# Performance work log

Measured on AMD Instinct MI355X. Metric: run time of the kernel, lower is better.

The kernel has to match this reference:

```python
import jax, jax.numpy as jnp
import numpy as np

T, B = 128, 512
IN = 512          # input_size = prod(observation_shape)
H = 1024          # hidden size
NA = 256          # n_actions
IDX0 = jnp.arange(0, 128)    # sub_indices[0]
IDX1 = jnp.arange(128, 256)  # sub_indices[1]


def _mlp(x, w1, b1, w2, b2, w3, b3):
    h = jnp.tanh(x @ w1.T + b1)
    h = jnp.tanh(h @ w2.T + b2)
    return h @ w3.T + b3


def _linear_init(key, out_dim, in_dim):
    kw, kb = jax.random.split(key)
    s = 1.0 / np.sqrt(in_dim)
    w = jax.random.uniform(kw, (out_dim, in_dim), jnp.float32, -s, s)
    b = jax.random.uniform(kb, (out_dim,), jnp.float32, -s, s)
    return w, b


def setup_inputs() -> dict:
    key = jax.random.key(0)
    ks = jax.random.split(key, 12)
    # observation: [T,B,IN+3]; last 3 dims are the routing gate features
    core = jax.random.normal(ks[0], (T, B, IN), jnp.float32)
    gate = jax.random.uniform(ks[1], (T, B, 3), jnp.float32, -0.2, 0.2)
    obs = jnp.concatenate([core, gate], axis=-1)
    pf_w1, pf_b1 = _linear_init(ks[2], H, IN)
    pf_w2, pf_b2 = _linear_init(ks[3], H, H)
    pf_w3, pf_b3 = _linear_init(ks[4], 128, H)
    pc_w1, pc_b1 = _linear_init(ks[5], H, IN)
    pc_w2, pc_b2 = _linear_init(ks[6], H, H)
    pc_w3, pc_b3 = _linear_init(ks[7], 128, H)
    v_w1, v_b1 = _linear_init(ks[8], H, IN)
    v_w2, v_b2 = _linear_init(ks[9], H, H)
    v_w3, v_b3 = _linear_init(ks[10], 1, H)
    return dict(
        observation=obs,
        prev_action=jnp.zeros((T, B), jnp.int32),
        prev_reward=jnp.zeros((T, B), jnp.float32),
        pf_w1=pf_w1, pf_b1=pf_b1, pf_w2=pf_w2, pf_b2=pf_b2, pf_w3=pf_w3, pf_b3=pf_b3,
        pc_w1=pc_w1, pc_b1=pc_b1, pc_w2=pc_w2, pc_b2=pc_b2, pc_w3=pc_w3, pc_b3=pc_b3,
        v_w1=v_w1, v_b1=v_b1, v_w2=v_w2, v_b2=v_b2, v_w3=v_w3, v_b3=v_b3,
    )


def reference(observation, prev_action, prev_reward,
              pf_w1, pf_b1, pf_w2, pf_b2, pf_w3, pf_b3,
              pc_w1, pc_b1, pc_w2, pc_b2, pc_w3, pc_b3,
              v_w1, v_b1, v_w2, v_b2, v_w3, v_b3):
    obs_flat = observation.reshape(T * B, -1)      # [TB, IN+3]
    x = obs_flat[:, :IN]                            # [TB, IN]
    # routing: free expert iff all 3 gate features have |.| <= 0.1
    mask = jnp.all(jnp.abs(obs_flat[:, IN:IN + 3]) <= 0.1, axis=-1)  # [TB]
    p_free = jax.nn.softmax(_mlp(x, pf_w1, pf_b1, pf_w2, pf_b2, pf_w3, pf_b3), axis=-1)
    p_con = jax.nn.softmax(_mlp(x, pc_w1, pc_b1, pc_w2, pc_b2, pc_w3, pc_b3), axis=-1)
    zeros = jnp.zeros((T * B, NA), x.dtype)
    pi_free = zeros.at[:, IDX0].set(p_free)
    pi_con = zeros.at[:, IDX1].set(p_con)
    pi = jnp.where(mask[:, None], pi_free, pi_con)  # [TB, NA]
    v = _mlp(x, v_w1, v_b1, v_w2, v_b2, v_w3, v_b3).squeeze(-1)  # [TB]
    return pi.reshape(T, B, NA), v.reshape(T, B)
```

## Files before the change

### kernel.cpp

```cpp
#include <hip/hip_runtime.h>
#include <stdint.h>

#define M_TOTAL 65536
#define IN_DIM 512
#define OBS_DIM 515

typedef __bf16 bf16x8 __attribute__((ext_vector_type(8)));
typedef float f32x4 __attribute__((ext_vector_type(4)));
typedef unsigned short u16x8 __attribute__((ext_vector_type(8)));

__device__ __forceinline__ unsigned short f2bf(float f) {
  unsigned u = __float_as_uint(f);
  u = (u + 0x7FFFu + ((u >> 16) & 1u)) >> 16;
  return (unsigned short)u;
}
__device__ __forceinline__ float bf2f(unsigned short h) {
  return __uint_as_float(((unsigned)h) << 16);
}
__device__ __forceinline__ float fast_tanh(float z) {
  float e = __expf(2.0f * z);
  return 1.0f - 2.0f / (e + 1.0f);
}
__device__ __forceinline__ void gl16(const void* g, void* l) {
  __builtin_amdgcn_global_load_lds(
      (__attribute__((address_space(1))) void*)g,
      (__attribute__((address_space(3))) void*)l, 16, 0, 0);
}

struct P8 { const float* p[8]; };

__global__ __launch_bounds__(256) void fused_cast(
    P8 srcs, unsigned short* __restrict__ dst, int* __restrict__ cnt) {
  if (blockIdx.x == 0 && threadIdx.x < 128) cnt[threadIdx.x] = 0;
  const int b0 = 524288, b1 = 1048576, b2 = 1572864, b3 = 2621440,
            b4 = 3670016, b5 = 4718592, b6 = 4849664, b7 = 4980736;
  int stride = gridDim.x * 256;
  for (int i = blockIdx.x * 256 + threadIdx.x; i < b7; i += stride) {
    const float* s; int off;
    if (i < b2)      { if (i < b0) { s = srcs.p[0]; off = i; }
                       else if (i < b1) { s = srcs.p[1]; off = i - b0; }
                       else { s = srcs.p[2]; off = i - b1; } }
    else if (i < b5) { if (i < b3) { s = srcs.p[3]; off = i - b2; }
                       else if (i < b4) { s = srcs.p[4]; off = i - b3; }
                       else { s = srcs.p[5]; off = i - b4; } }
    else             { if (i < b6) { s = srcs.p[6]; off = i - b5; }
                       else { s = srcs.p[7]; off = i - b6; } }
    dst[i] = f2bf(s[off]);
  }
}

__global__ __launch_bounds__(256) void compact_kernel(
    const float* __restrict__ obs,
    int* __restrict__ cntF, int* __restrict__ cntC,
    int* __restrict__ idxF, int* __restrict__ idxC, int C) {
  __shared__ int lcF, lcC, baseF, baseC;
  const int tid = threadIdx.x;
  const int r = blockIdx.x * 256 + tid;
  const float* g = obs + (size_t)r * OBS_DIM + IN_DIM;
  bool m = (fabsf(g[0]) <= 0.1f) && (fabsf(g[1]) <= 0.1f) && (fabsf(g[2]) <= 0.1f);
  if (tid == 0) { lcF = 0; lcC = 0; }
  __syncthreads();
  int slot = m ? atomicAdd(&lcF, 1) : atomicAdd(&lcC, 1);
  __syncthreads();
  const int c = r / C;
  if (tid == 0) {
    baseF = atomicAdd(&cntF[c], lcF);
    baseC = atomicAdd(&cntC[c], lcC);
  }
  __syncthreads();
  const int local = r - c * C;
  if (m) idxF[(size_t)c * C + baseF + slot] = local;
  else   idxC[(size_t)c * C + baseC + slot] = local;
}

__global__ __launch_bounds__(256) void build_idxP(
    const int* __restrict__ cntF, const int* __restrict__ cntC,
    const int* __restrict__ idxF, const int* __restrict__ idxC,
    int* __restrict__ idxP, int* __restrict__ meta, int C, int Cp) {
  const int bpc = Cp >> 8;
  const int c = blockIdx.x / bpc;
  const int i = (blockIdx.x % bpc) * 256 + threadIdx.x;
  const int cf = cntF[c], cc = cntC[c];
  const int padF = (cf + 127) & ~127;
  const int total = padF + ((cc + 127) & ~127);
  if ((blockIdx.x % bpc) == 0 && threadIdx.x == 0) {
    meta[2 * c] = padF; meta[2 * c + 1] = total;
  }
  if (i >= total) return;
  int v;
  if (i < padF) v = idxF[(size_t)c * C + (i < cf ? i : 0)];
  else { int j = i - padF; v = idxC[(size_t)c * C + (j < cc ? j : 0)]; }
  idxP[(size_t)c * Cp + i] = v;
}

__global__ __launch_bounds__(256) void prep_x(
    const float* __restrict__ obs, unsigned short* __restrict__ x, int row0) {
  int g = blockIdx.x * 256 + threadIdx.x;
  int row = g >> 9, col = g & 511;
  x[g] = f2bf(obs[(size_t)(row0 + row) * OBS_DIM + col]);
}

__global__ __launch_bounds__(256) void gemm_bt_tanh(
    const unsigned short* __restrict__ A, int lda,
    const unsigned short* __restrict__ B,
    const float* __restrict__ bias,
    unsigned short* __restrict__ Cmat, int ldc, int K)
{
  __shared__ alignas(16) unsigned short sA[128 * 32];
  __shared__ alignas(16) unsigned short sB[128 * 32];
  const int tid = threadIdx.x;
  const int nx = gridDim.x;
  const int nwg = nx * gridDim.y;
  const int orig = blockIdx.y * nx + blockIdx.x;
  const int wg = (orig & 7) * (nwg >> 3) + (orig >> 3);
  const int n0 = (wg % nx) << 7;
  const int m0 = (wg / nx) << 7;

  const int lane = tid & 63;
  const int wv = tid >> 6;
  const int wm = wv >> 1, wn = wv & 1;
  const int lr = lane & 15;
  const int lk = lane >> 4;

  const int ar0 = tid >> 2, ar1 = (256 + tid) >> 2;
  const int acol = (tid & 3) << 3;
  const unsigned short* Ap0 = A + (size_t)(m0 + ar0) * lda + acol;
  const unsigned short* Ap1 = A + (size_t)(m0 + ar1) * lda + acol;
  const unsigned short* Bp0 = B + (size_t)(n0 + ar0) * K + acol;
  const unsigned short* Bp1 = B + (size_t)(n0 + ar1) * K + acol;
  const int du = (tid & ~63) << 3;

  const f32x4 zero = {0.f, 0.f, 0.f, 0.f};
  f32x4 acc[4][4];
#pragma unroll
  for (int i = 0; i < 4; ++i)
#pragma unroll
    for (int j = 0; j < 4; ++j) acc[i][j] = zero;

  for (int kt = 0; kt < K; kt += 32) {
    __syncthreads();
    gl16(Ap0 + kt, &sA[du]);
    gl16(Bp0 + kt, &sB[du]);
    gl16(Ap1 + kt, &sA[du + 2048]);
    gl16(Bp1 + kt, &sB[du + 2048]);
    __syncthreads();
    bf16x8 af[4], bfr[4];
#pragma unroll
    for (int i = 0; i < 4; ++i)
      af[i] = *(const bf16x8*)&sA[((wm << 6) + (i << 4) + lr) * 32 + (lk << 3)];
#pragma unroll
    for (int j = 0; j < 4; ++j)
      bfr[j] = *(const bf16x8*)&sB[((wn << 6) + (j << 4) + lr) * 32 + (lk << 3)];
#pragma unroll
    for (int i = 0; i < 4; ++i)
#pragma unroll
      for (int j = 0; j < 4; ++j)
        acc[i][j] = __builtin_amdgcn_mfma_f32_16x16x32_bf16(af[i], bfr[j], acc[i][j], 0, 0, 0);
  }

  const int crow = m0 + (wm << 6);
  const int ccol = n0 + (wn << 6);
#pragma unroll
  for (int j = 0; j < 4; ++j) {
    int col = ccol + (j << 4) + lr;
    float bv = bias[col];
#pragma unroll
    for (int i = 0; i < 4; ++i) {
#pragma unroll
      for (int r = 0; r < 4; ++r) {
        int row = crow + (i << 4) + (lk << 2) + r;
        Cmat[(size_t)row * ldc + col] = f2bf(fast_tanh(acc[i][j][r] + bv));
      }
    }
  }
}

__global__ __launch_bounds__(256) void gemm_bt_tanh_p(
    const unsigned short* __restrict__ A, int lda,
    const unsigned short* __restrict__ BF, const unsigned short* __restrict__ BC,
    const float* __restrict__ biasF, const float* __restrict__ biasC,
    unsigned short* __restrict__ Cmat, int ldc, int K,
    const int* __restrict__ idxP, const int* __restrict__ meta)
{
  __shared__ alignas(16) unsigned short sA[128 * 32];
  __shared__ alignas(16) unsigned short sB[128 * 32];
  __shared__ int s_idx[128];
  const int tid = threadIdx.x;
  const int nx = gridDim.x;
  const int nwg = nx * gridDim.y;
  const int orig = blockIdx.y * nx + blockIdx.x;
  const int wg = (orig & 7) * (nwg >> 3) + (orig >> 3);
  const int n0 = (wg % nx) << 7;
  const int m0 = (wg / nx) << 7;

  const int padF = meta[0], total = meta[1];
  if (m0 >= total) return;
  const unsigned short* B = (m0 < padF) ? BF : BC;
  const float* bias = (m0 < padF) ? biasF : biasC;
  if (idxP && tid < 128) s_idx[tid] = idxP[m0 + tid];
  __syncthreads();

  const int lane = tid & 63;
  const int wv = tid >> 6;
  const int wm = wv >> 1, wn = wv & 1;
  const int lr = lane & 15;
  const int lk = lane >> 4;

  const int ar0 = tid >> 2, ar1 = (256 + tid) >> 2;
  const int acol = (tid & 3) << 3;
  const int ga0 = idxP ? s_idx[ar0] : (m0 + ar0);
  const int ga1 = idxP ? s_idx[ar1] : (m0 + ar1);
  const unsigned short* Ap0 = A + (size_t)ga0 * lda + acol;
  const unsigned short* Ap1 = A + (size_t)ga1 * lda + acol;
  const unsigned short* Bp0 = B + (size_t)(n0 + ar0) * K + acol;
  const unsigned short* Bp1 = B + (size_t)(n0 + ar1) * K + acol;
  const int du = (tid & ~63) << 3;

  const f32x4 zero = {0.f, 0.f, 0.f, 0.f};
  f32x4 acc[4][4];
#pragma unroll
  for (int i = 0; i < 4; ++i)
#pragma unroll
    for (int j = 0; j < 4; ++j) acc[i][j] = zero;

  for (int kt = 0; kt < K; kt += 32) {
    __syncthreads();
    gl16(Ap0 + kt, &sA[du]);
    gl16(Bp0 + kt, &sB[du]);
    gl16(Ap1 + kt, &sA[du + 2048]);
    gl16(Bp1 + kt, &sB[du + 2048]);
    __syncthreads();
    bf16x8 af[4], bfr[4];
#pragma unroll
    for (int i = 0; i < 4; ++i)
      af[i] = *(const bf16x8*)&sA[((wm << 6) + (i << 4) + lr) * 32 + (lk << 3)];
#pragma unroll
    for (int j = 0; j < 4; ++j)
      bfr[j] = *(const bf16x8*)&sB[((wn << 6) + (j << 4) + lr) * 32 + (lk << 3)];
#pragma unroll
    for (int i = 0; i < 4; ++i)
#pragma unroll
      for (int j = 0; j < 4; ++j)
        acc[i][j] = __builtin_amdgcn_mfma_f32_16x16x32_bf16(af[i], bfr[j], acc[i][j], 0, 0, 0);
  }

  const int crow = m0 + (wm << 6);
  const int ccol = n0 + (wn << 6);
#pragma unroll
  for (int j = 0; j < 4; ++j) {
    int col = ccol + (j << 4) + lr;
    float bv = bias[col];
#pragma unroll
    for (int i = 0; i < 4; ++i) {
#pragma unroll
      for (int r = 0; r < 4; ++r) {
        int row = crow + (i << 4) + (lk << 2) + r;
        Cmat[(size_t)row * ldc + col] = f2bf(fast_tanh(acc[i][j][r] + bv));
      }
    }
  }
}

__global__ __launch_bounds__(256) void l3_policy_p(
    const unsigned short* __restrict__ H2,
    const unsigned short* __restrict__ W3F, const unsigned short* __restrict__ W3C,
    const float* __restrict__ b3F, const float* __restrict__ b3C,
    const int* __restrict__ idxP, const int* __restrict__ meta,
    float* __restrict__ out_pi, int row0)
{
  __shared__ alignas(16) unsigned short sA[128 * 32];
  __shared__ alignas(16) unsigned short sB[128 * 32];
  __shared__ int s_idx[128];
  const int tid = threadIdx.x;
  const int m0 = blockIdx.x << 7;
  const int padF = meta[0], total = meta[1];
  if (m0 >= total) return;
  const bool freeg = (m0 < padF);
  const unsigned short* W3 = freeg ? W3F : W3C;
  const float* b3 = freeg ? b3F : b3C;
  const int half = freeg ? 0 : 128;
  if (tid < 128) s_idx[tid] = idxP[m0 + tid];
  __syncthreads();

  const int lane = tid & 63;
  const int wv = tid >> 6;
  const int lr = lane & 15;
  const int lk = lane >> 4;

  const int ar0 = tid >> 2, ar1 = (256 + tid) >> 2;
  const int acol = (tid & 3) << 3;
  const unsigned short* Ap0 = H2 + (size_t)(m0 + ar0) * 1024 + acol;
  const unsigned short* Ap1 = H2 + (size_t)(m0 + ar1) * 1024 + acol;
  const unsigned short* Bp0 = W3 + (size_t)ar0 * 1024 + acol;
  const unsigned short* Bp1 = W3 + (size_t)ar1 * 1024 + acol;
  const int du = (tid & ~63) << 3;

  const f32x4 zero = {0.f, 0.f, 0.f, 0.f};
  f32x4 acc[2][8];
#pragma unroll
  for (int i = 0; i < 2; ++i)
#pragma unroll
    for (int j = 0; j < 8; ++j) acc[i][j] = zero;

  for (int kt = 0; kt < 1024; kt += 32) {
    __syncthreads();
    gl16(Ap0 + kt, &sA[du]);
    gl16(Bp0 + kt, &sB[du]);
    gl16(Ap1 + kt, &sA[du + 2048]);
    gl16(Bp1 + kt, &sB[du + 2048]);
    __syncthreads();
    bf16x8 af[2], bfr[8];
#pragma unroll
    for (int i = 0; i < 2; ++i)
      af[i] = *(const bf16x8*)&sA[((wv << 5) + (i << 4) + lr) * 32 + (lk << 3)];
#pragma unroll
    for (int j = 0; j < 8; ++j)
      bfr[j] = *(const bf16x8*)&sB[((j << 4) + lr) * 32 + (lk << 3)];
#pragma unroll
    for (int i = 0; i < 2; ++i)
#pragma unroll
      for (int j = 0; j < 8; ++j)
        acc[i][j] = __builtin_amdgcn_mfma_f32_16x16x32_bf16(af[i], bfr[j], acc[i][j], 0, 0, 0);
  }

  float bv[8];
#pragma unroll
  for (int j = 0; j < 8; ++j) bv[j] = b3[(j << 4) + lr];

#pragma unroll
  for (int i = 0; i < 2; ++i) {
#pragma unroll
    for (int r = 0; r < 4; ++r) {
      float lg[8];
      float mx = -3.4e38f;
#pragma unroll
      for (int j = 0; j < 8; ++j) { lg[j] = acc[i][j][r] + bv[j]; mx = fmaxf(mx, lg[j]); }
#pragma unroll
      for (int d = 1; d < 16; d <<= 1) mx = fmaxf(mx, __shfl_xor(mx, d));
      float s = 0.f;
#pragma unroll
      for (int j = 0; j < 8; ++j) { lg[j] = __expf(lg[j] - mx); s += lg[j]; }
#pragma unroll
      for (int d = 1; d < 16; d <<= 1) s += __shfl_xor(s, d);
      float inv = 1.f / s;
      int compact = m0 + (wv << 5) + (i << 4) + (lk << 2) + r;
      int grow = row0 + s_idx[compact - m0];
      size_t base = (size_t)grow * 256;
#pragma unroll
      for (int j = 0; j < 8; ++j)
        out_pi[base + half + (j << 4) + lr] = lg[j] * inv;
#pragma unroll
      for (int j = 0; j < 8; ++j)
        out_pi[base + (half ^ 128) + (j << 4) + lr] = 0.0f;
    }
  }
}

__global__ __launch_bounds__(256) void l3_value(
    const unsigned short* __restrict__ H2,
    const float* __restrict__ w3,
    const float* __restrict__ b3,
    float* __restrict__ out_v, int row0, int C)
{
  const int lane = threadIdx.x & 63;
  const int row = (blockIdx.x << 2) + (threadIdx.x >> 6);
  if (row >= C) return;
  float s = 0.f;
#pragma unroll
  for (int it = 0; it < 2; ++it) {
    int k = (it << 9) + (lane << 3);
    u16x8 h = *(const u16x8*)(H2 + (size_t)row * 1024 + k);
    const float4* wp = (const float4*)(w3 + k);
    float4 w0 = wp[0], w1 = wp[1];
    s += bf2f(h[0]) * w0.x + bf2f(h[1]) * w0.y + bf2f(h[2]) * w0.z + bf2f(h[3]) * w0.w;
    s += bf2f(h[4]) * w1.x + bf2f(h[5]) * w1.y + bf2f(h[6]) * w1.z + bf2f(h[7]) * w1.w;
  }
#pragma unroll
  for (int d = 1; d < 64; d <<= 1) s += __shfl_xor(s, d);
  if (lane == 0) out_v[row0 + row] = s + b3[0];
}

extern "C" void kernel_launch(void* const* d_in, const int* in_sizes, int n_in,
                              void* d_out, int out_size, void* d_ws, size_t ws_size,
                              hipStream_t stream)
{
  (void)in_sizes; (void)n_in; (void)out_size;
  const float* obs   = (const float*)d_in[0];
  const float* pf_w1 = (const float*)d_in[3];
  const float* pf_b1 = (const float*)d_in[4];
  const float* pf_w2 = (const float*)d_in[5];
  const float* pf_b2 = (const float*)d_in[6];
  const float* pf_w3 = (const float*)d_in[7];
  const float* pf_b3 = (const float*)d_in[8];
  const float* pc_w1 = (const float*)d_in[9];
  const float* pc_b1 = (const float*)d_in[10];
  const float* pc_w2 = (const float*)d_in[11];
  const float* pc_b2 = (const float*)d_in[12];
  const float* pc_w3 = (const float*)d_in[13];
  const float* pc_b3 = (const float*)d_in[14];
  const float* v_w1  = (const float*)d_in[15];
  const float* v_b1  = (const float*)d_in[16];
  const float* v_w2  = (const float*)d_in[17];
  const float* v_b2  = (const float*)d_in[18];
  const float* v_w3  = (const float*)d_in[19];
  const float* v_b3  = (const float*)d_in[20];

  float* out_pi = (float*)d_out;
  float* out_v  = out_pi + (size_t)M_TOTAL * 256;

  char* ws = (char*)d_ws;
  unsigned short* wPF1 = (unsigned short*)ws;
  unsigned short* wPC1 = wPF1 + 524288;
  unsigned short* wV1  = wPC1 + 524288;
  unsigned short* wPF2 = wV1  + 524288;
  unsigned short* wPC2 = wPF2 + 1048576;
  unsigned short* wV2  = wPC2 + 1048576;
  unsigned short* wPF3 = wV2  + 1048576;
  unsigned short* wPC3 = wPF3 + 131072;
  int* cntF = (int*)(wPC3 + 131072);
  int* cntC = cntF + 64;
  int* idxF = cntC + 64;
  int* idxC = idxF + 65536;
  int* meta = idxC + 65536;
  int* idxP = meta + 128;
  unsigned short* xb = (unsigned short*)(idxP + 81920);

  const size_t fixed = (size_t)9961472 + 4 * (64 + 64 + 65536 + 65536 + 128 + 81920);
  int C = 1024;
  if      (ws_size >= fixed + 5120ull * 65536 + 1048576) C = 65536;
  else if (ws_size >= fixed + 5120ull * 32768 + 1048576) C = 32768;
  else if (ws_size >= fixed + 5120ull * 16384 + 1048576) C = 16384;
  else if (ws_size >= fixed + 5120ull *  8192 + 1048576) C = 8192;
  else if (ws_size >= fixed + 5120ull *  4096 + 1048576) C = 4096;
  else if (ws_size >= fixed + 5120ull *  2048 + 1048576) C = 2048;
  const int nchunk = M_TOTAL / C;
  const int Cp = C + 256;

  unsigned short* h1p = xb + (size_t)C * 512;
  unsigned short* h2p = h1p + (size_t)Cp * 1024;

  P8 srcs;
  srcs.p[0] = pf_w1; srcs.p[1] = pc_w1; srcs.p[2] = v_w1;
  srcs.p[3] = pf_w2; srcs.p[4] = pc_w2; srcs.p[5] = v_w2;
  srcs.p[6] = pf_w3; srcs.p[7] = pc_w3;
  fused_cast<<<2048, 256, 0, stream>>>(srcs, wPF1, cntF);
  compact_kernel<<<M_TOTAL / 256, 256, 0, stream>>>(obs, cntF, cntC, idxF, idxC, C);
  build_idxP<<<nchunk * (Cp / 256), 256, 0, stream>>>(cntF, cntC, idxF, idxC, idxP, meta, C, Cp);

  const dim3 gv(8, C / 128);
  const dim3 gp(8, Cp / 128);
  for (int c = 0; c < nchunk; ++c) {
    int row0 = c * C;
    prep_x<<<C * 512 / 256, 256, 0, stream>>>(obs, xb, row0);
    gemm_bt_tanh<<<gv, 256, 0, stream>>>(xb, 512, wV1, v_b1, h1p, 1024, 512);
    gemm_bt_tanh<<<gv, 256, 0, stream>>>(h1p, 1024, wV2, v_b2, h2p, 1024, 1024);
    l3_value<<<C / 4, 256, 0, stream>>>(h2p, v_w3, v_b3, out_v, row0, C);
    gemm_bt_tanh_p<<<gp, 256, 0, stream>>>(xb, 512, wPF1, wPC1, pf_b1, pc_b1,
                                           h1p, 1024, 512, idxP + (size_t)c * Cp, meta + 2 * c);
    gemm_bt_tanh_p<<<gp, 256, 0, stream>>>(h1p, 1024, wPF2, wPC2, pf_b2, pc_b2,
                                           h2p, 1024, 1024, nullptr, meta + 2 * c);
    l3_policy_p<<<Cp / 128, 256, 0, stream>>>(h2p, wPF3, wPC3, pf_b3, pc_b3,
                                              idxP + (size_t)c * Cp, meta + 2 * c, out_pi, row0);
  }
}
```

Baseline: 834.1 us.

## Replace 128x128 GEMMs with double-buffered 256x256 tile kernel using swizzled LDS

Both GEMM kernels are replaced by a single 512-thread kernel that computes 256x256 output tiles with a 64-wide K step. It double-buffers global-to-LDS loads across quarter-iterations, uses an XOR-swizzled LDS layout, and raises MFMA priority. Expert padding moves from 128 to 256 rows to match the larger tile. The aim is more data reuse per load and overlap of memory traffic with MFMA work. The cost is 128KB of LDS per block, which lowers occupancy, plus extra padded rows of wasted work.

```diff
diff --git a/kernel.cpp b/kernel.cpp
--- a/kernel.cpp
+++ b/kernel.cpp
@@ -81,8 +81,8 @@
   const int c = blockIdx.x / bpc;
   const int i = (blockIdx.x % bpc) * 256 + threadIdx.x;
   const int cf = cntF[c], cc = cntC[c];
-  const int padF = (cf + 127) & ~127;
-  const int total = padF + ((cc + 127) & ~127);
+  const int padF = (cf + 255) & ~255;
+  const int total = padF + ((cc + 255) & ~255);
   if ((blockIdx.x % bpc) == 0 && threadIdx.x == 0) {
     meta[2 * c] = padF; meta[2 * c + 1] = total;
   }
@@ -100,163 +100,157 @@
   x[g] = f2bf(obs[(size_t)(row0 + row) * OBS_DIM + col]);
 }
 
-__global__ __launch_bounds__(256) void gemm_bt_tanh(
-    const unsigned short* __restrict__ A, int lda,
-    const unsigned short* __restrict__ B,
-    const float* __restrict__ bias,
-    unsigned short* __restrict__ Cmat, int ldc, int K)
-{
-  __shared__ alignas(16) unsigned short sA[128 * 32];
-  __shared__ alignas(16) unsigned short sB[128 * 32];
-  const int tid = threadIdx.x;
-  const int nx = gridDim.x;
-  const int nwg = nx * gridDim.y;
-  const int orig = blockIdx.y * nx + blockIdx.x;
-  const int wg = (orig & 7) * (nwg >> 3) + (orig >> 3);
-  const int n0 = (wg % nx) << 7;
-  const int m0 = (wg / nx) << 7;
-
-  const int lane = tid & 63;
-  const int wv = tid >> 6;
-  const int wm = wv >> 1, wn = wv & 1;
-  const int lr = lane & 15;
-  const int lk = lane >> 4;
-
-  const int ar0 = tid >> 2, ar1 = (256 + tid) >> 2;
-  const int acol = (tid & 3) << 3;
-  const unsigned short* Ap0 = A + (size_t)(m0 + ar0) * lda + acol;
-  const unsigned short* Ap1 = A + (size_t)(m0 + ar1) * lda + acol;
-  const unsigned short* Bp0 = B + (size_t)(n0 + ar0) * K + acol;
-  const unsigned short* Bp1 = B + (size_t)(n0 + ar1) * K + acol;
-  const int du = (tid & ~63) << 3;
-
-  const f32x4 zero = {0.f, 0.f, 0.f, 0.f};
-  f32x4 acc[4][4];
-#pragma unroll
-  for (int i = 0; i < 4; ++i)
-#pragma unroll
-    for (int j = 0; j < 4; ++j) acc[i][j] = zero;
-
-  for (int kt = 0; kt < K; kt += 32) {
-    __syncthreads();
-    gl16(Ap0 + kt, &sA[du]);
-    gl16(Bp0 + kt, &sB[du]);
-    gl16(Ap1 + kt, &sA[du + 2048]);
-    gl16(Bp1 + kt, &sB[du + 2048]);
-    __syncthreads();
-    bf16x8 af[4], bfr[4];
-#pragma unroll
-    for (int i = 0; i < 4; ++i)
-      af[i] = *(const bf16x8*)&sA[((wm << 6) + (i << 4) + lr) * 32 + (lk << 3)];
-#pragma unroll
-    for (int j = 0; j < 4; ++j)
-      bfr[j] = *(const bf16x8*)&sB[((wn << 6) + (j << 4) + lr) * 32 + (lk << 3)];
-#pragma unroll
-    for (int i = 0; i < 4; ++i)
-#pragma unroll
-      for (int j = 0; j < 4; ++j)
-        acc[i][j] = __builtin_amdgcn_mfma_f32_16x16x32_bf16(af[i], bfr[j], acc[i][j], 0, 0, 0);
-  }
-
-  const int crow = m0 + (wm << 6);
-  const int ccol = n0 + (wn << 6);
-#pragma unroll
-  for (int j = 0; j < 4; ++j) {
-    int col = ccol + (j << 4) + lr;
-    float bv = bias[col];
-#pragma unroll
-    for (int i = 0; i < 4; ++i) {
-#pragma unroll
-      for (int r = 0; r < 4; ++r) {
-        int row = crow + (i << 4) + (lk << 2) + r;
-        Cmat[(size_t)row * ldc + col] = f2bf(fast_tanh(acc[i][j][r] + bv));
-      }
-    }
-  }
-}
-
-__global__ __launch_bounds__(256) void gemm_bt_tanh_p(
+#define STAGE_A(h, tt, db) { \
+    const unsigned short* _s = pA[h] + (size_t)(tt) * 64 + grp8; \
+    char* _d = smem + (db) * 65536 + (h) * 16384 + wbase; \
+    gl16(_s, _d); gl16(_s + 32, _d + 8192); }
+#define STAGE_B(h, tt, db) { \
+    const unsigned short* _s = pB[h] + (size_t)(tt) * 64 + grp8; \
+    char* _d = smem + (db) * 65536 + 32768 + (h) * 16384 + wbase; \
+    gl16(_s, _d); gl16(_s + 32, _d + 8192); }
+
+__global__ __launch_bounds__(512) void gemm256(
     const unsigned short* __restrict__ A, int lda,
     const unsigned short* __restrict__ BF, const unsigned short* __restrict__ BC,
     const float* __restrict__ biasF, const float* __restrict__ biasC,
     unsigned short* __restrict__ Cmat, int ldc, int K,
-    const int* __restrict__ idxP, const int* __restrict__ meta)
+    const int* __restrict__ idxP, const int* __restrict__ meta, int Mrows)
 {
-  __shared__ alignas(16) unsigned short sA[128 * 32];
-  __shared__ alignas(16) unsigned short sB[128 * 32];
-  __shared__ int s_idx[128];
+  extern __shared__ char smem[];
   const int tid = threadIdx.x;
-  const int nx = gridDim.x;
-  const int nwg = nx * gridDim.y;
-  const int orig = blockIdx.y * nx + blockIdx.x;
-  const int wg = (orig & 7) * (nwg >> 3) + (orig >> 3);
-  const int n0 = (wg % nx) << 7;
-  const int m0 = (wg / nx) << 7;
-
-  const int padF = meta[0], total = meta[1];
+
+  const int nwg = gridDim.x * gridDim.y;
+  const int orig = blockIdx.y * gridDim.x + blockIdx.x;
+  const int qq = nwg >> 3, rr = nwg & 7, xc = orig & 7, oo = orig >> 3;
+  const int wg = (xc < rr ? xc * (qq + 1) : rr * (qq + 1) + (xc - rr) * qq) + oo;
+  const int n0 = (wg % gridDim.x) << 8;
+  const int m0 = (wg / gridDim.x) << 8;
+
+  const int padF  = meta ? meta[0] : (1 << 30);
+  const int total = meta ? meta[1] : Mrows;
   if (m0 >= total) return;
   const unsigned short* B = (m0 < padF) ? BF : BC;
   const float* bias = (m0 < padF) ? biasF : biasC;
-  if (idxP && tid < 128) s_idx[tid] = idxP[m0 + tid];
-  __syncthreads();
 
   const int lane = tid & 63;
   const int wv = tid >> 6;
-  const int wm = wv >> 1, wn = wv & 1;
+  const int wm = wv >> 2, wn = wv & 3;
   const int lr = lane & 15;
   const int lk = lane >> 4;
 
-  const int ar0 = tid >> 2, ar1 = (256 + tid) >> 2;
-  const int acol = (tid & 3) << 3;
-  const int ga0 = idxP ? s_idx[ar0] : (m0 + ar0);
-  const int ga1 = idxP ? s_idx[ar1] : (m0 + ar1);
-  const unsigned short* Ap0 = A + (size_t)ga0 * lda + acol;
-  const unsigned short* Ap1 = A + (size_t)ga1 * lda + acol;
-  const unsigned short* Bp0 = B + (size_t)(n0 + ar0) * K + acol;
-  const unsigned short* Bp1 = B + (size_t)(n0 + ar1) * K + acol;
-  const int du = (tid & ~63) << 3;
+  const int srow = tid >> 2;
+  const int grp8 = (((tid & 3) ^ ((srow >> 1) & 3)) << 3);
+  const int wbase = (tid & ~63) << 4;
+  const unsigned short* pA[2];
+  const unsigned short* pB[2];
+#pragma unroll
+  for (int h = 0; h < 2; ++h) {
+    int gr = m0 + h * 128 + srow;
+    int ga = idxP ? idxP[gr] : gr;
+    pA[h] = A + (size_t)ga * lda;
+    pB[h] = B + (size_t)(n0 + h * 128 + srow) * K;
+  }
+
+  int a_off[4], b_off[2];
+#pragma unroll
+  for (int f = 0; f < 4; ++f) {
+    int hr = wm * 64 + f * 16 + lr;
+    a_off[f] = hr * 64 + ((lk ^ ((hr >> 1) & 3)) << 4);
+  }
+#pragma unroll
+  for (int g = 0; g < 2; ++g) {
+    int hb = wn * 32 + g * 16 + lr;
+    b_off[g] = hb * 64 + ((lk ^ ((hb >> 1) & 3)) << 4);
+  }
 
   const f32x4 zero = {0.f, 0.f, 0.f, 0.f};
-  f32x4 acc[4][4];
-#pragma unroll
-  for (int i = 0; i < 4; ++i)
+  f32x4 acc[8][4];
+#pragma unroll
+  for (int i = 0; i < 8; ++i)
 #pragma unroll
     for (int j = 0; j < 4; ++j) acc[i][j] = zero;
 
-  for (int kt = 0; kt < K; kt += 32) {
-    __syncthreads();
-    gl16(Ap0 + kt, &sA[du]);
-    gl16(Bp0 + kt, &sB[du]);
-    gl16(Ap1 + kt, &sA[du + 2048]);
-    gl16(Bp1 + kt, &sB[du + 2048]);
-    __syncthreads();
-    bf16x8 af[4], bfr[4];
-#pragma unroll
-    for (int i = 0; i < 4; ++i)
-      af[i] = *(const bf16x8*)&sA[((wm << 6) + (i << 4) + lr) * 32 + (lk << 3)];
-#pragma unroll
-    for (int j = 0; j < 4; ++j)
-      bfr[j] = *(const bf16x8*)&sB[((wn << 6) + (j << 4) + lr) * 32 + (lk << 3)];
-#pragma unroll
-    for (int i = 0; i < 4; ++i)
-#pragma unroll
-      for (int j = 0; j < 4; ++j)
-        acc[i][j] = __builtin_amdgcn_mfma_f32_16x16x32_bf16(af[i], bfr[j], acc[i][j], 0, 0, 0);
-  }
-
-  const int crow = m0 + (wm << 6);
-  const int ccol = n0 + (wn << 6);
-#pragma unroll
-  for (int j = 0; j < 4; ++j) {
-    int col = ccol + (j << 4) + lr;
+  const int NT = K >> 6;
+  STAGE_A(0, 0, 0); STAGE_B(0, 0, 0); STAGE_A(1, 0, 0); STAGE_B(1, 0, 0);
+  STAGE_A(0, 1, 1); STAGE_B(0, 1, 1);
+  asm volatile("s_waitcnt vmcnt(4)" ::: "memory");
+  __builtin_amdgcn_s_barrier();
+
+  bf16x8 a[4][2], b0[2][2], b1[2][2];
+  for (int T = 0; T < NT; ++T) {
+    const int b = T & 1;
+    const int tt1 = (T + 1 < NT) ? T + 1 : NT - 1;
+    const int tt2 = (T + 2 < NT) ? T + 2 : NT - 1;
+#pragma unroll
+    for (int q = 0; q < 4; ++q) {
+      const int mh = q >> 1, nh = q & 1;
+      if (q == 0) {
+        const char* Ab = smem + b * 65536;
+        const char* Bb = smem + b * 65536 + 32768;
+#pragma unroll
+        for (int f = 0; f < 4; ++f)
+#pragma unroll
+          for (int kk = 0; kk < 2; ++kk)
+            a[f][kk] = *(const bf16x8*)(Ab + kk * 8192 + a_off[f]);
+#pragma unroll
+        for (int g = 0; g < 2; ++g)
+#pragma unroll
+          for (int kk = 0; kk < 2; ++kk)
+            b0[g][kk] = *(const bf16x8*)(Bb + kk * 8192 + b_off[g]);
+      } else if (q == 1) {
+        const char* Bb = smem + b * 65536 + 32768 + 16384;
+#pragma unroll
+        for (int g = 0; g < 2; ++g)
+#pragma unroll
+          for (int kk = 0; kk < 2; ++kk)
+            b1[g][kk] = *(const bf16x8*)(Bb + kk * 8192 + b_off[g]);
+      } else if (q == 2) {
+        const char* Ab = smem + b * 65536 + 16384;
+#pragma unroll
+        for (int f = 0; f < 4; ++f)
+#pragma unroll
+          for (int kk = 0; kk < 2; ++kk)
+            a[f][kk] = *(const bf16x8*)(Ab + kk * 8192 + a_off[f]);
+      }
+      if (q == 0)      { STAGE_A(1, tt1, b ^ 1); }
+      else if (q == 1) { STAGE_B(1, tt1, b ^ 1); }
+      else if (q == 2) { STAGE_A(0, tt2, b); }
+      else             { STAGE_B(0, tt2, b); }
+      __builtin_amdgcn_s_barrier();
+      asm volatile("s_waitcnt lgkmcnt(0)" ::: "memory");
+      __builtin_amdgcn_sched_barrier(0);
+      __builtin_amdgcn_s_setprio(1);
+#pragma unroll
+      for (int f = 0; f < 4; ++f)
+#pragma unroll
+        for (int g = 0; g < 2; ++g)
+#pragma unroll
+          for (int kk = 0; kk < 2; ++kk) {
+            if (nh == 0)
+              acc[mh * 4 + f][g] = __builtin_amdgcn_mfma_f32_16x16x32_bf16(
+                  a[f][kk], b0[g][kk], acc[mh * 4 + f][g], 0, 0, 0);
+            else
+              acc[mh * 4 + f][2 + g] = __builtin_amdgcn_mfma_f32_16x16x32_bf16(
+                  a[f][kk], b1[g][kk], acc[mh * 4 + f][2 + g], 0, 0, 0);
+          }
+      __builtin_amdgcn_s_setprio(0);
+      if (q == 3) asm volatile("s_waitcnt vmcnt(4)" ::: "memory");
+      __builtin_amdgcn_s_barrier();
+    }
+  }
+
+#pragma unroll
+  for (int N = 0; N < 4; ++N) {
+    const int nh = N >> 1, g = N & 1;
+    int col = n0 + nh * 128 + wn * 32 + g * 16 + lr;
     float bv = bias[col];
 #pragma unroll
-    for (int i = 0; i < 4; ++i) {
-#pragma unroll
-      for (int r = 0; r < 4; ++r) {
-        int row = crow + (i << 4) + (lk << 2) + r;
-        Cmat[(size_t)row * ldc + col] = f2bf(fast_tanh(acc[i][j][r] + bv));
-      }
+    for (int M = 0; M < 8; ++M) {
+      const int mh = M >> 2, f = M & 3;
+      int rowb = m0 + mh * 128 + wm * 64 + f * 16 + lk * 4;
+#pragma unroll
+      for (int r = 0; r < 4; ++r)
+        Cmat[(size_t)(rowb + r) * ldc + col] = f2bf(fast_tanh(acc[M][N][r] + bv));
     }
   }
 }
@@ -427,17 +421,20 @@
 
   const size_t fixed = (size_t)9961472 + 4 * (64 + 64 + 65536 + 65536 + 128 + 81920);
   int C = 1024;
-  if      (ws_size >= fixed + 5120ull * 65536 + 1048576) C = 65536;
-  else if (ws_size >= fixed + 5120ull * 32768 + 1048576) C = 32768;
-  else if (ws_size >= fixed + 5120ull * 16384 + 1048576) C = 16384;
-  else if (ws_size >= fixed + 5120ull *  8192 + 1048576) C = 8192;
-  else if (ws_size >= fixed + 5120ull *  4096 + 1048576) C = 4096;
-  else if (ws_size >= fixed + 5120ull *  2048 + 1048576) C = 2048;
+  if      (ws_size >= fixed + 5120ull * 65536 + 3145728) C = 65536;
+  else if (ws_size >= fixed + 5120ull * 32768 + 3145728) C = 32768;
+  else if (ws_size >= fixed + 5120ull * 16384 + 3145728) C = 16384;
+  else if (ws_size >= fixed + 5120ull *  8192 + 3145728) C = 8192;
+  else if (ws_size >= fixed + 5120ull *  4096 + 3145728) C = 4096;
+  else if (ws_size >= fixed + 5120ull *  2048 + 3145728) C = 2048;
   const int nchunk = M_TOTAL / C;
-  const int Cp = C + 256;
+  const int Cp = C + 512;
 
   unsigned short* h1p = xb + (size_t)C * 512;
   unsigned short* h2p = h1p + (size_t)Cp * 1024;
+
+  (void)hipFuncSetAttribute((const void*)gemm256,
+      hipFuncAttributeMaxDynamicSharedMemorySize, 131072);
 
   P8 srcs;
   srcs.p[0] = pf_w1; srcs.p[1] = pc_w1; srcs.p[2] = v_w1;
@@ -447,18 +444,20 @@
   compact_kernel<<<M_TOTAL / 256, 256, 0, stream>>>(obs, cntF, cntC, idxF, idxC, C);
   build_idxP<<<nchunk * (Cp / 256), 256, 0, stream>>>(cntF, cntC, idxF, idxC, idxP, meta, C, Cp);
 
-  const dim3 gv(8, C / 128);
-  const dim3 gp(8, Cp / 128);
+  const dim3 gv(4, C / 256);
+  const dim3 gp(4, Cp / 256);
   for (int c = 0; c < nchunk; ++c) {
     int row0 = c * C;
     prep_x<<<C * 512 / 256, 256, 0, stream>>>(obs, xb, row0);
-    gemm_bt_tanh<<<gv, 256, 0, stream>>>(xb, 512, wV1, v_b1, h1p, 1024, 512);
-    gemm_bt_tanh<<<gv, 256, 0, stream>>>(h1p, 1024, wV2, v_b2, h2p, 1024, 1024);
+    gemm256<<<gv, 512, 131072, stream>>>(xb, 512, wV1, wV1, v_b1, v_b1,
+                                         h1p, 1024, 512, nullptr, nullptr, C);
+    gemm256<<<gv, 512, 131072, stream>>>(h1p, 1024, wV2, wV2, v_b2, v_b2,
+                                         h2p, 1024, 1024, nullptr, nullptr, C);
     l3_value<<<C / 4, 256, 0, stream>>>(h2p, v_w3, v_b3, out_v, row0, C);
-    gemm_bt_tanh_p<<<gp, 256, 0, stream>>>(xb, 512, wPF1, wPC1, pf_b1, pc_b1,
-                                           h1p, 1024, 512, idxP + (size_t)c * Cp, meta + 2 * c);
-    gemm_bt_tanh_p<<<gp, 256, 0, stream>>>(h1p, 1024, wPF2, wPC2, pf_b2, pc_b2,
-                                           h2p, 1024, 1024, nullptr, meta + 2 * c);
+    gemm256<<<gp, 512, 131072, stream>>>(xb, 512, wPF1, wPC1, pf_b1, pc_b1,
+                                         h1p, 1024, 512, idxP + (size_t)c * Cp, meta + 2 * c, 0);
+    gemm256<<<gp, 512, 131072, stream>>>(h1p, 1024, wPF2, wPC2, pf_b2, pc_b2,
+                                         h2p, 1024, 1024, nullptr, meta + 2 * c, 0);
     l3_policy_p<<<Cp / 128, 256, 0, stream>>>(h2p, wPF3, wPC3, pf_b3, pc_b3,
                                               idxP + (size_t)c * Cp, meta + 2 * c, out_pi, row0);
   }
```

Measured after the change: 725.9 us. 1.15x faster.
